# Kernel tuning notes

Measured on AMD Instinct MI355X. Metric: run time of the kernel, lower is better.

## Reference

```python
import jax, jax.numpy as jnp
import numpy as np

N = 65536      # total voxels (lidar + image tokens)
D = 256        # d_model
H = 8          # nhead
DFF = 2048     # dim_feedforward
SS = 128       # set_size
SN = 512       # set_num (SN * SS == N, each partition is a permutation of all voxels)
NSHIFT = 2


def setup_inputs() -> dict:
    key = jax.random.key(0)
    ks = jax.random.split(key, 10)
    src = jax.random.normal(ks[0], (N, D), jnp.float32)
    pos_embed = jax.random.normal(ks[1], (NSHIFT, N, D), jnp.float32) * 0.02
    # each (shift, set_id) partition covers every voxel exactly once
    inds = jnp.stack([
        jnp.stack([
            jax.random.permutation(jax.random.fold_in(ks[2], s * 2 + p), N).reshape(SN, SS)
            for p in range(2)
        ])
        for s in range(NSHIFT)
    ]).astype(jnp.int32)                      # (NSHIFT, 2, SN, SS)
    masks = jax.random.uniform(ks[3], (NSHIFT, 2, SN, SS)) < 0.1
    masks = masks.at[..., 0].set(False)       # keep at least one key per set
    init = lambda k, shape: jax.random.normal(k, shape, jnp.float32) * 0.02
    return {
        'src': src, 'pos_embed': pos_embed,
        'set_voxel_inds': inds, 'set_voxel_masks': masks,
        'w_qkv': init(ks[4], (2, 3 * D, D)), 'b_qkv': jnp.zeros((2, 3 * D)),
        'w_out': init(ks[5], (2, D, D)), 'b_out': jnp.zeros((2, D)),
        'w_ff1': init(ks[6], (2, DFF, D)), 'b_ff1': jnp.zeros((2, DFF)),
        'w_ff2': init(ks[7], (2, D, DFF)), 'b_ff2': jnp.zeros((2, D)),
        'g_n1': jnp.ones((2, D)), 'b_n1': jnp.zeros((2, D)),
        'g_n2': jnp.ones((2, D)), 'b_n2': jnp.zeros((2, D)),
        'g_ln': jnp.ones((2, D)), 'b_ln': jnp.zeros((2, D)),
    }


def _ln(x, g, b):
    m = jnp.mean(x, -1, keepdims=True)
    v = jnp.mean(jnp.square(x - m), -1, keepdims=True)
    return (x - m) * jax.lax.rsqrt(v + 1e-5) * g + b


def _mha(q_in, k_in, v_in, mask, wqkv, bqkv, wo, bo):
    # q_in/k_in/v_in: (SN, SS, D); mask: (SN, SS) True = ignore key
    wq, wk, wv = jnp.split(wqkv, 3, axis=0)
    bq, bk, bv = jnp.split(bqkv, 3, axis=0)
    hd = D // H
    q = (q_in @ wq.T + bq).reshape(SN, SS, H, hd)
    k = (k_in @ wk.T + bk).reshape(SN, SS, H, hd)
    v = (v_in @ wv.T + bv).reshape(SN, SS, H, hd)
    scores = jnp.einsum('bqhd,bkhd->bhqk', q, k) / np.float32(np.sqrt(hd))
    scores = jnp.where(mask[:, None, None, :], jnp.float32(-1e9), scores)
    attn = jax.nn.softmax(scores, axis=-1)
    o = jnp.einsum('bhqk,bkhd->bqhd', attn, v).reshape(SN, SS, D)
    return o @ wo.T + bo


def reference(src, pos_embed, set_voxel_inds, set_voxel_masks,
              w_qkv, b_qkv, w_out, b_out, w_ff1, b_ff1, w_ff2, b_ff2,
              g_n1, b_n1, g_n2, b_n2, g_ln, b_ln):
    out = src
    set_id = 0  # block_id % 2 with block_id == 0
    for i in range(NSHIFT):  # two encoder layers, one per shift
        inds = set_voxel_inds[i, set_id]   # (SN, SS)
        mask = set_voxel_masks[i, set_id]  # (SN, SS)
        pos = pos_embed[i]
        identity = out
        feat = out[inds]                   # gather voxels into sets
        qk = feat + pos[inds]
        a = _mha(qk, qk, feat, mask, w_qkv[i], b_qkv[i], w_out[i], b_out[i])
        # scatter back: per voxel, take its FIRST occurrence in flattened set order
        flat = inds.reshape(-1)
        L = flat.shape[0]
        perm = jnp.full((N,), L, jnp.int32).at[flat].min(jnp.arange(L, dtype=jnp.int32))
        src2 = a.reshape(-1, D)[perm]
        x = _ln(out + src2, g_n1[i], b_n1[i])
        ff = jax.nn.relu(x @ w_ff1[i].T + b_ff1[i]) @ w_ff2[i].T + b_ff2[i]
        x = _ln(x + ff, g_n2[i], b_n2[i])
        out = _ln(x + identity, g_ln[i], b_ln[i])
    return out
```

## Files before the change

kernel.cpp:

```cpp
#include <hip/hip_runtime.h>
#include <math.h>

#define NVOX 65536
#define DM 256
#define NH 8
#define HDIM 32
#define DFFN 2048
#define SSZ 128
#define SNUM 512

#define AS1 __attribute__((address_space(1)))
#define AS3 __attribute__((address_space(3)))

typedef __attribute__((ext_vector_type(8))) __bf16 bf16x8;
typedef __attribute__((ext_vector_type(8))) unsigned short u16x8;
typedef __attribute__((ext_vector_type(4))) float f32x4;

__device__ __forceinline__ unsigned short f2bf(float f) {
    unsigned int u = __float_as_uint(f);
    u += 0x7fffu + ((u >> 16) & 1u);
    return (unsigned short)(u >> 16);
}
__device__ __forceinline__ float bf2f(unsigned short u) {
    return __uint_as_float(((unsigned int)u) << 16);
}

__global__ __launch_bounds__(256)
void cvt_bf16_kernel(const float* __restrict__ in, unsigned short* __restrict__ out, int n) {
    int i = blockIdx.x * 256 + threadIdx.x;
    int stride = gridDim.x * 256;
    for (; i < n; i += stride) out[i] = f2bf(in[i]);
}

__global__ __launch_bounds__(256)
void gather_kernel(const float* __restrict__ src, const float* __restrict__ pos,
                   const int* __restrict__ inds,
                   unsigned short* __restrict__ qk, unsigned short* __restrict__ feat) {
    int j = blockIdx.x * 4 + (threadIdx.x >> 6);
    int lane = threadIdx.x & 63;
    int v = inds[j];
    float4 a = ((const float4*)(src + (size_t)v * DM))[lane];
    float4 p = ((const float4*)(pos + (size_t)v * DM))[lane];
    ushort4 qo, fo;
    qo.x = f2bf(a.x + p.x); qo.y = f2bf(a.y + p.y);
    qo.z = f2bf(a.z + p.z); qo.w = f2bf(a.w + p.w);
    fo.x = f2bf(a.x); fo.y = f2bf(a.y); fo.z = f2bf(a.z); fo.w = f2bf(a.w);
    ((ushort4*)(qk   + (size_t)j * DM))[lane] = qo;
    ((ushort4*)(feat + (size_t)j * DM))[lane] = fo;
}

#define VMCNT4 asm volatile("s_waitcnt vmcnt(4)" ::: "memory")
#define VMCNT0 asm volatile("s_waitcnt vmcnt(0)" ::: "memory")

template<bool RELU, bool OBF16>
__global__ __launch_bounds__(512)
void gemm_mfma256(const unsigned short* __restrict__ A, const unsigned short* __restrict__ W,
                  const float* __restrict__ bias, void* __restrict__ Cout,
                  int M, int N, int K) {
    __shared__ alignas(16) char smem[69632];
    unsigned short* As = (unsigned short*)smem;
    unsigned short* Bs = (unsigned short*)(smem + 32768);
    float* ebuf = (float*)smem;
    const int ES = 264;

    int tid = threadIdx.x;
    int wave = tid >> 6, lane = tid & 63;
    int wm = wave >> 2;
    int wn = wave & 3;
    int mBase = blockIdx.x * 256, nBase = blockIdx.y * 256;

    int rr = lane & 15;
    int kq = (lane >> 4) * 8;
    int rbase = (lane >> 4) * 4;

    f32x4 acc[8][4];
    const f32x4 zero = {0.f, 0.f, 0.f, 0.f};
#pragma unroll
    for (int m = 0; m < 8; m++)
#pragma unroll
        for (int n = 0; n < 4; n++) acc[m][n] = zero;

    const unsigned short* gA0 = A + (size_t)(mBase + (wave * 2 + 0) * 16 + rr) * K + kq;
    const unsigned short* gA1 = A + (size_t)(mBase + (wave * 2 + 1) * 16 + rr) * K + kq;
    const unsigned short* gB0 = W + (size_t)(nBase + (wave * 2 + 0) * 16 + rr) * K + kq;
    const unsigned short* gB1 = W + (size_t)(nBase + (wave * 2 + 1) * 16 + rr) * K + kq;

    auto stage = [&](int b, int kt) {
        int ko = kt * 32;
        __builtin_amdgcn_global_load_lds((const AS1 void*)(gA0 + ko),
            (AS3 void*)(As + b * 8192 + (wave * 2 + 0) * 512), 16, 0, 0);
        __builtin_amdgcn_global_load_lds((const AS1 void*)(gA1 + ko),
            (AS3 void*)(As + b * 8192 + (wave * 2 + 1) * 512), 16, 0, 0);
        __builtin_amdgcn_global_load_lds((const AS1 void*)(gB0 + ko),
            (AS3 void*)(Bs + b * 8192 + (wave * 2 + 0) * 512), 16, 0, 0);
        __builtin_amdgcn_global_load_lds((const AS1 void*)(gB1 + ko),
            (AS3 void*)(Bs + b * 8192 + (wave * 2 + 1) * 512), 16, 0, 0);
    };

    int nt = K >> 5;
    stage(0, 0);

    for (int t = 0; t < nt; ++t) {
        int p = t & 1;
        if (t + 1 < nt) {
            stage(p ^ 1, t + 1);
            VMCNT4;
        } else {
            VMCNT0;
        }
        __builtin_amdgcn_s_barrier();
        __builtin_amdgcn_sched_barrier(0);

        bf16x8 af[8], bf[4];
#pragma unroll
        for (int m = 0; m < 8; m++)
            af[m] = *(const bf16x8*)(As + p * 8192 + (wm * 8 + m) * 512 + lane * 8);
#pragma unroll
        for (int n = 0; n < 4; n++)
            bf[n] = *(const bf16x8*)(Bs + p * 8192 + (wn * 4 + n) * 512 + lane * 8);
#pragma unroll
        for (int m = 0; m < 8; m++)
#pragma unroll
            for (int n = 0; n < 4; n++)
                acc[m][n] = __builtin_amdgcn_mfma_f32_16x16x32_bf16(af[m], bf[n], acc[m][n], 0, 0, 0);

        __builtin_amdgcn_sched_barrier(0);
        __builtin_amdgcn_s_barrier();
    }

    float bn[4];
#pragma unroll
    for (int n = 0; n < 4; n++)
        bn[n] = bias[nBase + wn * 64 + n * 16 + rr];

    int erow = tid >> 3;
    int ec0  = (tid & 7) * 32;
#pragma unroll
    for (int pass = 0; pass < 4; ++pass) {
        __syncthreads();
        if (wm == (pass >> 1)) {
#pragma unroll
            for (int mm = 0; mm < 4; ++mm) {
                int m = (pass & 1) * 4 + mm;
#pragma unroll
                for (int n = 0; n < 4; ++n) {
                    int lcol = wn * 64 + n * 16 + rr;
#pragma unroll
                    for (int r = 0; r < 4; ++r) {
                        float v = acc[m][n][r] + bn[n];
                        if (RELU) v = fmaxf(v, 0.f);
                        ebuf[(mm * 16 + rbase + r) * ES + lcol] = v;
                    }
                }
            }
        }
        __syncthreads();
        int grow = mBase + pass * 64 + erow;
        if (OBF16) {
            unsigned short* dst = (unsigned short*)Cout + (size_t)grow * N + nBase + ec0;
#pragma unroll
            for (int g = 0; g < 4; ++g) {
                u16x8 o;
#pragma unroll
                for (int j = 0; j < 8; ++j)
                    o[j] = f2bf(ebuf[erow * ES + ec0 + g * 8 + j]);
                *(u16x8*)(dst + g * 8) = o;
            }
        } else {
            float* dst = (float*)Cout + (size_t)grow * N + nBase + ec0;
#pragma unroll
            for (int g = 0; g < 8; ++g)
                *(float4*)(dst + g * 4) = *(float4*)(ebuf + erow * ES + ec0 + g * 4);
        }
    }
}

__global__ __launch_bounds__(256)
void attn_mfma_kernel(const unsigned short* __restrict__ QK,
                      const unsigned short* __restrict__ V,
                      const unsigned char* __restrict__ mask,
                      unsigned short* __restrict__ ao) {
    int s = blockIdx.x, h = blockIdx.y;
    int tid = threadIdx.x;
    int wq = tid >> 6;
    int lane = tid & 63;

    __shared__ alignas(16) unsigned short Ks[128 * 40];
    __shared__ alignas(16) unsigned short Vt[32 * 136];
    __shared__ alignas(16) unsigned short Plds[4 * 4096];
    __shared__ unsigned char msk[SSZ];

#pragma unroll
    for (int it = 0; it < 2; it++) {
        int idx = tid + it * 256;
        int key = idx >> 2, dimoff = (idx & 3) * 8;
        bf16x8 kv = *(const bf16x8*)(QK + (size_t)(s * SSZ + key) * 512 + 256 + h * HDIM + dimoff);
        *(bf16x8*)(Ks + key * 40 + dimoff) = kv;
        u16x8 vv = *(const u16x8*)(V + (size_t)(s * SSZ + key) * DM + h * HDIM + dimoff);
#pragma unroll
        for (int j = 0; j < 8; j++) Vt[(dimoff + j) * 136 + key] = vv[j];
    }
    if (tid < SSZ) msk[tid] = mask[s * SSZ + tid];
    __syncthreads();

    int rr = lane & 15;
    int kq = (lane >> 4) * 8;
    const f32x4 zero = {0.f, 0.f, 0.f, 0.f};

    bf16x8 qa[2];
#pragma unroll
    for (int mt = 0; mt < 2; mt++)
        qa[mt] = *(const bf16x8*)(QK + (size_t)(s * SSZ + wq * 32 + mt * 16 + rr) * 512 + h * HDIM + kq);

    f32x4 S[2][8];
#pragma unroll
    for (int nt = 0; nt < 8; nt++) {
        bf16x8 kb = *(const bf16x8*)(Ks + (nt * 16 + rr) * 40 + kq);
#pragma unroll
        for (int mt = 0; mt < 2; mt++)
            S[mt][nt] = __builtin_amdgcn_mfma_f32_16x16x32_bf16(qa[mt], kb, zero, 0, 0, 0);
    }

    const float SCALE = 0.17677669529663687f;
    f32x4 rm[2];
#pragma unroll
    for (int mt = 0; mt < 2; mt++) { rm[mt].x = rm[mt].y = rm[mt].z = rm[mt].w = -1e30f; }
#pragma unroll
    for (int nt = 0; nt < 8; nt++) {
        bool mv = msk[nt * 16 + rr] != 0;
#pragma unroll
        for (int mt = 0; mt < 2; mt++) {
#pragma unroll
            for (int r = 0; r < 4; r++) {
                float v = mv ? -1e30f : S[mt][nt][r] * SCALE;
                S[mt][nt][r] = v;
                rm[mt][r] = fmaxf(rm[mt][r], v);
            }
        }
    }
#pragma unroll
    for (int off = 1; off < 16; off <<= 1) {
#pragma unroll
        for (int mt = 0; mt < 2; mt++)
#pragma unroll
            for (int r = 0; r < 4; r++)
                rm[mt][r] = fmaxf(rm[mt][r], __shfl_xor(rm[mt][r], off));
    }

    f32x4 rs[2];
#pragma unroll
    for (int mt = 0; mt < 2; mt++) { rs[mt] = zero; }
#pragma unroll
    for (int nt = 0; nt < 8; nt++)
#pragma unroll
        for (int mt = 0; mt < 2; mt++)
#pragma unroll
            for (int r = 0; r < 4; r++) {
                float p = __expf(S[mt][nt][r] - rm[mt][r]);
                S[mt][nt][r] = p;
                rs[mt][r] += p;
            }
#pragma unroll
    for (int off = 1; off < 16; off <<= 1) {
#pragma unroll
        for (int mt = 0; mt < 2; mt++)
#pragma unroll
            for (int r = 0; r < 4; r++)
                rs[mt][r] += __shfl_xor(rs[mt][r], off);
    }

    char* Pbase = (char*)Plds + wq * 8192;
#pragma unroll
    for (int nt = 0; nt < 8; nt++)
#pragma unroll
        for (int mt = 0; mt < 2; mt++)
#pragma unroll
            for (int r = 0; r < 4; r++) {
                int prow = mt * 16 + (lane >> 4) * 4 + r;
                int col  = nt * 16 + rr;
                unsigned addr = (unsigned)(prow * 256 + col * 2) ^ ((prow & 7) << 4);
                *(unsigned short*)(Pbase + addr) = f2bf(S[mt][nt][r]);
            }
    __syncthreads();

    f32x4 O[2][2];
#pragma unroll
    for (int mt = 0; mt < 2; mt++)
#pragma unroll
        for (int nd = 0; nd < 2; nd++) O[mt][nd] = zero;
#pragma unroll
    for (int kc = 0; kc < 4; kc++) {
        bf16x8 pa[2];
#pragma unroll
        for (int mt = 0; mt < 2; mt++) {
            int prow = mt * 16 + rr;
            unsigned addr = (unsigned)(prow * 256 + (kc * 32 + kq) * 2) ^ ((prow & 7) << 4);
            pa[mt] = *(const bf16x8*)(Pbase + addr);
        }
#pragma unroll
        for (int nd = 0; nd < 2; nd++) {
            bf16x8 vb = *(const bf16x8*)(Vt + (nd * 16 + rr) * 136 + kc * 32 + kq);
#pragma unroll
            for (int mt = 0; mt < 2; mt++)
                O[mt][nd] = __builtin_amdgcn_mfma_f32_16x16x32_bf16(pa[mt], vb, O[mt][nd], 0, 0, 0);
        }
    }

#pragma unroll
    for (int mt = 0; mt < 2; mt++) {
#pragma unroll
        for (int nd = 0; nd < 2; nd++) {
#pragma unroll
            for (int r = 0; r < 4; r++) {
                int row = s * SSZ + wq * 32 + mt * 16 + (lane >> 4) * 4 + r;
                int col = h * HDIM + nd * 16 + rr;
                ao[(size_t)row * DM + col] = f2bf(O[mt][nd][r] / rs[mt][r]);
            }
        }
    }
}

__device__ inline float4 ln4(float4 t, int lane, const float* __restrict__ g,
                             const float* __restrict__ b) {
    float s = t.x + t.y + t.z + t.w;
    float s2 = t.x * t.x + t.y * t.y + t.z * t.z + t.w * t.w;
#pragma unroll
    for (int off = 32; off; off >>= 1) {
        s += __shfl_xor(s, off);
        s2 += __shfl_xor(s2, off);
    }
    float mean = s * (1.0f / 256.0f);
    float var = fmaf(-mean, mean, s2 * (1.0f / 256.0f));
    float rs = rsqrtf(var + 1e-5f);
    float4 g4 = ((const float4*)g)[lane];
    float4 b4 = ((const float4*)b)[lane];
    float4 o;
    o.x = fmaf((t.x - mean) * rs, g4.x, b4.x);
    o.y = fmaf((t.y - mean) * rs, g4.y, b4.y);
    o.z = fmaf((t.z - mean) * rs, g4.z, b4.z);
    o.w = fmaf((t.w - mean) * rs, g4.w, b4.w);
    return o;
}

__global__ __launch_bounds__(256)
void scatter_ln_kernel(const unsigned short* __restrict__ a, const int* __restrict__ inds,
                       const float* __restrict__ prev,
                       const float* __restrict__ g, const float* __restrict__ b,
                       float* __restrict__ x, unsigned short* __restrict__ x_bf) {
    int j = blockIdx.x * 4 + (threadIdx.x >> 6);
    int lane = threadIdx.x & 63;
    int v = inds[j];
    ushort4 av = ((const ushort4*)(a + (size_t)j * DM))[lane];
    float4 pv = ((const float4*)(prev + (size_t)v * DM))[lane];
    float4 t = make_float4(bf2f(av.x) + pv.x, bf2f(av.y) + pv.y,
                           bf2f(av.z) + pv.z, bf2f(av.w) + pv.w);
    float4 o = ln4(t, lane, g, b);
    ((float4*)(x + (size_t)v * DM))[lane] = o;
    ushort4 ob;
    ob.x = f2bf(o.x); ob.y = f2bf(o.y); ob.z = f2bf(o.z); ob.w = f2bf(o.w);
    ((ushort4*)(x_bf + (size_t)v * DM))[lane] = ob;
}

__global__ __launch_bounds__(256)
void final_ln_kernel(const float* __restrict__ x, const float* __restrict__ y,
                     const float* __restrict__ prev,
                     const float* __restrict__ g2, const float* __restrict__ b2,
                     const float* __restrict__ gl, const float* __restrict__ bl,
                     float* __restrict__ out) {
    int v = blockIdx.x * 4 + (threadIdx.x >> 6);
    int lane = threadIdx.x & 63;
    size_t base = (size_t)v * DM;
    float4 xv = ((const float4*)(x + base))[lane];
    float4 yv = ((const float4*)(y + base))[lane];
    float4 t = make_float4(xv.x + yv.x, xv.y + yv.y, xv.z + yv.z, xv.w + yv.w);
    float4 t2 = ln4(t, lane, g2, b2);
    float4 pv = ((const float4*)(prev + base))[lane];
    float4 u = make_float4(t2.x + pv.x, t2.y + pv.y, t2.z + pv.z, t2.w + pv.w);
    float4 o = ln4(u, lane, gl, bl);
    ((float4*)(out + base))[lane] = o;
}

extern "C" void kernel_launch(void* const* d_in, const int* in_sizes, int n_in,
                              void* d_out, int out_size, void* d_ws, size_t ws_size,
                              hipStream_t stream) {
    const float* src       = (const float*)d_in[0];
    const float* pos_embed = (const float*)d_in[1];
    const int*   inds_all  = (const int*)d_in[2];
    const unsigned char* masks_all = (const unsigned char*)d_in[3];
    const float* w_qkv = (const float*)d_in[4];
    const float* b_qkv = (const float*)d_in[5];
    const float* w_out = (const float*)d_in[6];
    const float* b_out = (const float*)d_in[7];
    const float* w_ff1 = (const float*)d_in[8];
    const float* b_ff1 = (const float*)d_in[9];
    const float* w_ff2 = (const float*)d_in[10];
    const float* b_ff2 = (const float*)d_in[11];
    const float* g_n1 = (const float*)d_in[12];
    const float* b_n1 = (const float*)d_in[13];
    const float* g_n2 = (const float*)d_in[14];
    const float* b_n2 = (const float*)d_in[15];
    const float* g_ln = (const float*)d_in[16];
    const float* b_ln = (const float*)d_in[17];
    float* out = (float*)d_out;

    const size_t NVF = (size_t)NVOX * DM;
    unsigned short* A = (unsigned short*)d_ws;
    unsigned short* B = A + NVF;
    unsigned short* C = B + NVF;
    unsigned short* D = C + 2 * NVF;
    float* F = (float*)(D + NVF);
    unsigned short* wts = (unsigned short*)(F + NVF);
    const size_t SZ_QKV = (size_t)2 * 3 * DM * DM;
    const size_t SZ_WO  = (size_t)2 * DM * DM;
    const size_t SZ_FF1 = (size_t)2 * DFFN * DM;
    const size_t SZ_FF2 = (size_t)2 * DM * DFFN;
    unsigned short* wqkv_bf = wts;
    unsigned short* wo_bf   = wqkv_bf + SZ_QKV;
    unsigned short* wff1_bf = wo_bf + SZ_WO;
    unsigned short* wff2_bf = wff1_bf + SZ_FF1;
    unsigned short* hbuf    = wff2_bf + SZ_FF2;

    size_t used_bytes = (char*)hbuf - (char*)d_ws;
    long long avail = (long long)ws_size - (long long)used_bytes;
    long long crows = avail / (DFFN * 2);
    if (crows > NVOX) crows = NVOX;
    crows &= ~255LL;
    int chunk = (crows < 256) ? 256 : (int)crows;

    cvt_bf16_kernel<<<512, 256, 0, stream>>>(w_qkv, wqkv_bf, (int)SZ_QKV);
    cvt_bf16_kernel<<<256, 256, 0, stream>>>(w_out, wo_bf, (int)SZ_WO);
    cvt_bf16_kernel<<<1024, 256, 0, stream>>>(w_ff1, wff1_bf, (int)SZ_FF1);
    cvt_bf16_kernel<<<1024, 256, 0, stream>>>(w_ff2, wff2_bf, (int)SZ_FF2);

    for (int i = 0; i < 2; i++) {
        const float* prev = (i == 0) ? src : out;
        const int* inds = inds_all + (size_t)i * 2 * SNUM * SSZ;
        const unsigned char* mask = masks_all + (size_t)i * 2 * SNUM * SSZ;
        const float* pos  = pos_embed + (size_t)i * NVF;
        const unsigned short* wqkv = wqkv_bf + (size_t)i * 3 * DM * DM;
        const unsigned short* wo   = wo_bf + (size_t)i * DM * DM;
        const unsigned short* wff1 = wff1_bf + (size_t)i * DFFN * DM;
        const unsigned short* wff2 = wff2_bf + (size_t)i * DM * DFFN;
        const float* bqkv = b_qkv + (size_t)i * 3 * DM;
        const float* bo   = b_out + (size_t)i * DM;
        const float* bff1 = b_ff1 + (size_t)i * DFFN;
        const float* bff2 = b_ff2 + (size_t)i * DM;

        gather_kernel<<<NVOX / 4, 256, 0, stream>>>(prev, pos, inds, A, B);

        gemm_mfma256<false, true><<<dim3(NVOX / 256, 512 / 256), 512, 0, stream>>>(
            A, wqkv, bqkv, C, NVOX, 512, DM);
        gemm_mfma256<false, true><<<dim3(NVOX / 256, 1), 512, 0, stream>>>(
            B, wqkv + (size_t)512 * DM, bqkv + 512, D, NVOX, DM, DM);

        attn_mfma_kernel<<<dim3(SNUM, NH), 256, 0, stream>>>(C, D, mask, A);

        gemm_mfma256<false, true><<<dim3(NVOX / 256, 1), 512, 0, stream>>>(
            A, wo, bo, C, NVOX, DM, DM);

        scatter_ln_kernel<<<NVOX / 4, 256, 0, stream>>>(
            C, inds, prev, g_n1 + i * DM, b_n1 + i * DM, F, B);

        float* y = (float*)C;
        for (int r0 = 0; r0 < NVOX; r0 += chunk) {
            int rows = (NVOX - r0 < chunk) ? (NVOX - r0) : chunk;
            gemm_mfma256<true, true><<<dim3(rows / 256, DFFN / 256), 512, 0, stream>>>(
                B + (size_t)r0 * DM, wff1, bff1, hbuf, rows, DFFN, DM);
            gemm_mfma256<false, false><<<dim3(rows / 256, 1), 512, 0, stream>>>(
                hbuf, wff2, bff2, y + (size_t)r0 * DM, rows, DM, DFFN);
        }

        final_ln_kernel<<<NVOX / 4, 256, 0, stream>>>(
            F, y, prev, g_n2 + i * DM, b_n2 + i * DM,
            g_ln + i * DM, b_ln + i * DM, out);
    }
}
```

Measured before the change: 1.188 ms.

## Fuse scatter+LayerNorm and final double LayerNorm into GEMM epilogues, swizzle blocks

The GEMM template gains epilogue modes. The output-projection GEMM now gathers the residual by index, applies LayerNorm and scatters fp32 and bf16 results in place. The FF2 GEMM now does the residual add plus both LayerNorms and writes the layer output directly. This removes the separate scatter_ln and final_ln kernels and their extra full-tensor memory round trips. A workgroup-index swizzle is added to improve cache locality, and the FFN chunk size is rounded to multiples of 2048. The cost is higher register pressure and longer epilogues inside the GEMM.

```diff
diff --git a/kernel.cpp b/kernel.cpp
--- a/kernel.cpp
+++ b/kernel.cpp
@@ -52,11 +52,16 @@
 #define VMCNT4 asm volatile("s_waitcnt vmcnt(4)" ::: "memory")
 #define VMCNT0 asm volatile("s_waitcnt vmcnt(0)" ::: "memory")
 
-template<bool RELU, bool OBF16>
+template<int EPI, bool RELU>
 __global__ __launch_bounds__(512)
 void gemm_mfma256(const unsigned short* __restrict__ A, const unsigned short* __restrict__ W,
                   const float* __restrict__ bias, void* __restrict__ Cout,
-                  int M, int N, int K) {
+                  int M, int N, int K,
+                  const int* __restrict__ inds,
+                  const float* __restrict__ res1, const float* __restrict__ res2,
+                  const float* __restrict__ g1, const float* __restrict__ b1,
+                  const float* __restrict__ g2, const float* __restrict__ b2,
+                  unsigned short* __restrict__ out2) {
     __shared__ alignas(16) char smem[69632];
     unsigned short* As = (unsigned short*)smem;
     unsigned short* Bs = (unsigned short*)(smem + 32768);
@@ -67,7 +72,14 @@
     int wave = tid >> 6, lane = tid & 63;
     int wm = wave >> 2;
     int wn = wave & 3;
-    int mBase = blockIdx.x * 256, nBase = blockIdx.y * 256;
+
+    unsigned lin = blockIdx.x + blockIdx.y * gridDim.x;
+    unsigned nwg = gridDim.x * gridDim.y;
+    unsigned swz = lin;
+    if ((nwg & 7u) == 0u) { unsigned cpx = nwg >> 3; swz = (lin & 7u) * cpx + (lin >> 3); }
+    int bx = (int)(swz / gridDim.y);
+    int by = (int)(swz % gridDim.y);
+    int mBase = bx * 256, nBase = by * 256;
 
     int rr = lane & 15;
     int kq = (lane >> 4) * 8;
@@ -156,7 +168,8 @@
         }
         __syncthreads();
         int grow = mBase + pass * 64 + erow;
-        if (OBF16) {
+
+        if constexpr (EPI == 0) {
             unsigned short* dst = (unsigned short*)Cout + (size_t)grow * N + nBase + ec0;
 #pragma unroll
             for (int g = 0; g < 4; ++g) {
@@ -166,11 +179,96 @@
                     o[j] = f2bf(ebuf[erow * ES + ec0 + g * 8 + j]);
                 *(u16x8*)(dst + g * 8) = o;
             }
-        } else {
+        } else if constexpr (EPI == 1) {
             float* dst = (float*)Cout + (size_t)grow * N + nBase + ec0;
 #pragma unroll
             for (int g = 0; g < 8; ++g)
                 *(float4*)(dst + g * 4) = *(float4*)(ebuf + erow * ES + ec0 + g * 4);
+        } else if constexpr (EPI == 2) {
+            int v = inds[grow];
+            const float* pr = res1 + (size_t)v * 256;
+            f32x4 tv[8];
+            float s = 0.f, s2 = 0.f;
+#pragma unroll
+            for (int g = 0; g < 8; ++g) {
+                float4 e = *(float4*)(ebuf + erow * ES + ec0 + g * 4);
+                float4 p = *(const float4*)(pr + ec0 + g * 4);
+                f32x4 t = {e.x + p.x, e.y + p.y, e.z + p.z, e.w + p.w};
+                tv[g] = t;
+                s += t[0] + t[1] + t[2] + t[3];
+                s2 += t[0]*t[0] + t[1]*t[1] + t[2]*t[2] + t[3]*t[3];
+            }
+#pragma unroll
+            for (int off = 1; off < 8; off <<= 1) { s += __shfl_xor(s, off); s2 += __shfl_xor(s2, off); }
+            float mean = s * (1.f/256.f);
+            float var = fmaf(-mean, mean, s2 * (1.f/256.f));
+            float rs = rsqrtf(var + 1e-5f);
+            float* xd = (float*)Cout + (size_t)v * 256 + ec0;
+            unsigned short* xb = out2 + (size_t)v * 256 + ec0;
+#pragma unroll
+            for (int g = 0; g < 8; ++g) {
+                float4 gg = *(const float4*)(g1 + ec0 + g * 4);
+                float4 bb = *(const float4*)(b1 + ec0 + g * 4);
+                float4 o;
+                o.x = fmaf((tv[g][0] - mean) * rs, gg.x, bb.x);
+                o.y = fmaf((tv[g][1] - mean) * rs, gg.y, bb.y);
+                o.z = fmaf((tv[g][2] - mean) * rs, gg.z, bb.z);
+                o.w = fmaf((tv[g][3] - mean) * rs, gg.w, bb.w);
+                *(float4*)(xd + g * 4) = o;
+                ushort4 ob; ob.x = f2bf(o.x); ob.y = f2bf(o.y); ob.z = f2bf(o.z); ob.w = f2bf(o.w);
+                *(ushort4*)(xb + g * 4) = ob;
+            }
+        } else {
+            const float* xr = res2 + (size_t)grow * 256;
+            const float* pr = res1 + (size_t)grow * 256;
+            f32x4 tv[8];
+            float s = 0.f, s2 = 0.f;
+#pragma unroll
+            for (int g = 0; g < 8; ++g) {
+                float4 e = *(float4*)(ebuf + erow * ES + ec0 + g * 4);
+                float4 x = *(const float4*)(xr + ec0 + g * 4);
+                f32x4 t = {e.x + x.x, e.y + x.y, e.z + x.z, e.w + x.w};
+                tv[g] = t;
+                s += t[0] + t[1] + t[2] + t[3];
+                s2 += t[0]*t[0] + t[1]*t[1] + t[2]*t[2] + t[3]*t[3];
+            }
+#pragma unroll
+            for (int off = 1; off < 8; off <<= 1) { s += __shfl_xor(s, off); s2 += __shfl_xor(s2, off); }
+            float mean = s * (1.f/256.f);
+            float var = fmaf(-mean, mean, s2 * (1.f/256.f));
+            float rs = rsqrtf(var + 1e-5f);
+            float s3 = 0.f, s4 = 0.f;
+#pragma unroll
+            for (int g = 0; g < 8; ++g) {
+                float4 gg = *(const float4*)(g1 + ec0 + g * 4);
+                float4 bb = *(const float4*)(b1 + ec0 + g * 4);
+                float4 p = *(const float4*)(pr + ec0 + g * 4);
+                f32x4 u;
+                u[0] = fmaf((tv[g][0] - mean) * rs, gg.x, bb.x) + p.x;
+                u[1] = fmaf((tv[g][1] - mean) * rs, gg.y, bb.y) + p.y;
+                u[2] = fmaf((tv[g][2] - mean) * rs, gg.z, bb.z) + p.z;
+                u[3] = fmaf((tv[g][3] - mean) * rs, gg.w, bb.w) + p.w;
+                tv[g] = u;
+                s3 += u[0] + u[1] + u[2] + u[3];
+                s4 += u[0]*u[0] + u[1]*u[1] + u[2]*u[2] + u[3]*u[3];
+            }
+#pragma unroll
+            for (int off = 1; off < 8; off <<= 1) { s3 += __shfl_xor(s3, off); s4 += __shfl_xor(s4, off); }
+            float mean2 = s3 * (1.f/256.f);
+            float var2 = fmaf(-mean2, mean2, s4 * (1.f/256.f));
+            float rs2 = rsqrtf(var2 + 1e-5f);
+            float* od = (float*)Cout + (size_t)grow * 256 + ec0;
+#pragma unroll
+            for (int g = 0; g < 8; ++g) {
+                float4 gg = *(const float4*)(g2 + ec0 + g * 4);
+                float4 bb = *(const float4*)(b2 + ec0 + g * 4);
+                float4 o;
+                o.x = fmaf((tv[g][0] - mean2) * rs2, gg.x, bb.x);
+                o.y = fmaf((tv[g][1] - mean2) * rs2, gg.y, bb.y);
+                o.z = fmaf((tv[g][2] - mean2) * rs2, gg.z, bb.z);
+                o.w = fmaf((tv[g][3] - mean2) * rs2, gg.w, bb.w);
+                *(float4*)(od + g * 4) = o;
+            }
         }
     }
 }
@@ -318,66 +416,6 @@
             }
         }
     }
-}
-
-__device__ inline float4 ln4(float4 t, int lane, const float* __restrict__ g,
-                             const float* __restrict__ b) {
-    float s = t.x + t.y + t.z + t.w;
-    float s2 = t.x * t.x + t.y * t.y + t.z * t.z + t.w * t.w;
-#pragma unroll
-    for (int off = 32; off; off >>= 1) {
-        s += __shfl_xor(s, off);
-        s2 += __shfl_xor(s2, off);
-    }
-    float mean = s * (1.0f / 256.0f);
-    float var = fmaf(-mean, mean, s2 * (1.0f / 256.0f));
-    float rs = rsqrtf(var + 1e-5f);
-    float4 g4 = ((const float4*)g)[lane];
-    float4 b4 = ((const float4*)b)[lane];
-    float4 o;
-    o.x = fmaf((t.x - mean) * rs, g4.x, b4.x);
-    o.y = fmaf((t.y - mean) * rs, g4.y, b4.y);
-    o.z = fmaf((t.z - mean) * rs, g4.z, b4.z);
-    o.w = fmaf((t.w - mean) * rs, g4.w, b4.w);
-    return o;
-}
-
-__global__ __launch_bounds__(256)
-void scatter_ln_kernel(const unsigned short* __restrict__ a, const int* __restrict__ inds,
-                       const float* __restrict__ prev,
-                       const float* __restrict__ g, const float* __restrict__ b,
-                       float* __restrict__ x, unsigned short* __restrict__ x_bf) {
-    int j = blockIdx.x * 4 + (threadIdx.x >> 6);
-    int lane = threadIdx.x & 63;
-    int v = inds[j];
-    ushort4 av = ((const ushort4*)(a + (size_t)j * DM))[lane];
-    float4 pv = ((const float4*)(prev + (size_t)v * DM))[lane];
-    float4 t = make_float4(bf2f(av.x) + pv.x, bf2f(av.y) + pv.y,
-                           bf2f(av.z) + pv.z, bf2f(av.w) + pv.w);
-    float4 o = ln4(t, lane, g, b);
-    ((float4*)(x + (size_t)v * DM))[lane] = o;
-    ushort4 ob;
-    ob.x = f2bf(o.x); ob.y = f2bf(o.y); ob.z = f2bf(o.z); ob.w = f2bf(o.w);
-    ((ushort4*)(x_bf + (size_t)v * DM))[lane] = ob;
-}
-
-__global__ __launch_bounds__(256)
-void final_ln_kernel(const float* __restrict__ x, const float* __restrict__ y,
-                     const float* __restrict__ prev,
-                     const float* __restrict__ g2, const float* __restrict__ b2,
-                     const float* __restrict__ gl, const float* __restrict__ bl,
-                     float* __restrict__ out) {
-    int v = blockIdx.x * 4 + (threadIdx.x >> 6);
-    int lane = threadIdx.x & 63;
-    size_t base = (size_t)v * DM;
-    float4 xv = ((const float4*)(x + base))[lane];
-    float4 yv = ((const float4*)(y + base))[lane];
-    float4 t = make_float4(xv.x + yv.x, xv.y + yv.y, xv.z + yv.z, xv.w + yv.w);
-    float4 t2 = ln4(t, lane, g2, b2);
-    float4 pv = ((const float4*)(prev + base))[lane];
-    float4 u = make_float4(t2.x + pv.x, t2.y + pv.y, t2.z + pv.z, t2.w + pv.w);
-    float4 o = ln4(u, lane, gl, bl);
-    ((float4*)(out + base))[lane] = o;
 }
 
 extern "C" void kernel_launch(void* const* d_in, const int* in_sizes, int n_in,
@@ -424,8 +462,8 @@
     long long avail = (long long)ws_size - (long long)used_bytes;
     long long crows = avail / (DFFN * 2);
     if (crows > NVOX) crows = NVOX;
-    crows &= ~255LL;
-    int chunk = (crows < 256) ? 256 : (int)crows;
+    crows &= ~2047LL;
+    int chunk = (crows < 2048) ? 2048 : (int)crows;
 
     cvt_bf16_kernel<<<512, 256, 0, stream>>>(w_qkv, wqkv_bf, (int)SZ_QKV);
     cvt_bf16_kernel<<<256, 256, 0, stream>>>(w_out, wo_bf, (int)SZ_WO);
@@ -448,30 +486,28 @@
 
         gather_kernel<<<NVOX / 4, 256, 0, stream>>>(prev, pos, inds, A, B);
 
-        gemm_mfma256<false, true><<<dim3(NVOX / 256, 512 / 256), 512, 0, stream>>>(
-            A, wqkv, bqkv, C, NVOX, 512, DM);
-        gemm_mfma256<false, true><<<dim3(NVOX / 256, 1), 512, 0, stream>>>(
-            B, wqkv + (size_t)512 * DM, bqkv + 512, D, NVOX, DM, DM);
+        gemm_mfma256<0, false><<<dim3(NVOX / 256, 512 / 256), 512, 0, stream>>>(
+            A, wqkv, bqkv, C, NVOX, 512, DM,
+            nullptr, nullptr, nullptr, nullptr, nullptr, nullptr, nullptr, nullptr);
+        gemm_mfma256<0, false><<<dim3(NVOX / 256, 1), 512, 0, stream>>>(
+            B, wqkv + (size_t)512 * DM, bqkv + 512, D, NVOX, DM, DM,
+            nullptr, nullptr, nullptr, nullptr, nullptr, nullptr, nullptr, nullptr);
 
         attn_mfma_kernel<<<dim3(SNUM, NH), 256, 0, stream>>>(C, D, mask, A);
 
-        gemm_mfma256<false, true><<<dim3(NVOX / 256, 1), 512, 0, stream>>>(
-            A, wo, bo, C, NVOX, DM, DM);
-
-        scatter_ln_kernel<<<NVOX / 4, 256, 0, stream>>>(
-            C, inds, prev, g_n1 + i * DM, b_n1 + i * DM, F, B);
-
-        float* y = (float*)C;
+        gemm_mfma256<2, false><<<dim3(NVOX / 256, 1), 512, 0, stream>>>(
+            A, wo, bo, F, NVOX, DM, DM,
+            inds, prev, nullptr, g_n1 + i * DM, b_n1 + i * DM, nullptr, nullptr, B);
+
         for (int r0 = 0; r0 < NVOX; r0 += chunk) {
             int rows = (NVOX - r0 < chunk) ? (NVOX - r0) : chunk;
-            gemm_mfma256<true, true><<<dim3(rows / 256, DFFN / 256), 512, 0, stream>>>(
-                B + (size_t)r0 * DM, wff1, bff1, hbuf, rows, DFFN, DM);
-            gemm_mfma256<false, false><<<dim3(rows / 256, 1), 512, 0, stream>>>(
-                hbuf, wff2, bff2, y + (size_t)r0 * DM, rows, DM, DFFN);
-        }
-
-        final_ln_kernel<<<NVOX / 4, 256, 0, stream>>>(
-            F, y, prev, g_n2 + i * DM, b_n2 + i * DM,
-            g_ln + i * DM, b_ln + i * DM, out);
-    }
-}
+            gemm_mfma256<0, true><<<dim3(rows / 256, DFFN / 256), 512, 0, stream>>>(
+                B + (size_t)r0 * DM, wff1, bff1, hbuf, rows, DFFN, DM,
+                nullptr, nullptr, nullptr, nullptr, nullptr, nullptr, nullptr, nullptr);
+            gemm_mfma256<3, false><<<dim3(rows / 256, 1), 512, 0, stream>>>(
+                hbuf, wff2, bff2, out + (size_t)r0 * DM, rows, DM, DFFN,
+                nullptr, prev + (size_t)r0 * DM, F + (size_t)r0 * DM,
+                g_n2 + i * DM, b_n2 + i * DM, g_ln + i * DM, b_ln + i * DM, nullptr);
+        }
+    }
+}
```

Measured after the change: 1.173 ms. About the same (-1.2%).
